# Optimization experiments

Hardware: AMD Instinct MI355X
Metric: run time of the kernel (lower is better)

Reference implementation:

```python
import jax, jax.numpy as jnp
import numpy as np

N_NODES = 100000
N_EDGES = 1600000
IN_FEATS = 128
H_FEATS = 64
NUM_CLASSES = 40
NEG_SLOPE = 0.2  # DGL GATConv default


def gat_layer(x, src, dst, W, attn_l, attn_r, bias, n_nodes):
    # x: [N, din]; W: [din, dout]; attn_l/r, bias: [dout]
    feat = x @ W                                   # [N, dout]
    el = feat @ attn_l                             # [N]
    er = feat @ attn_r                             # [N]
    e = jax.nn.leaky_relu(el[src] + er[dst], NEG_SLOPE)  # [E]
    # segment softmax over destination nodes (numerically stable)
    m = jax.ops.segment_max(e, dst, num_segments=n_nodes)   # [N]
    ee = jnp.exp(e - m[dst])                                 # [E]
    s = jax.ops.segment_sum(ee, dst, num_segments=n_nodes)  # [N]
    alpha = ee / s[dst]                                      # [E]
    out = jax.ops.segment_sum(alpha[:, None] * feat[src], dst,
                              num_segments=n_nodes)          # [N, dout]
    return out + bias


def setup_inputs() -> dict:
    key = jax.random.key(0)
    ks = jax.random.split(key, 12)
    in_feat = jax.random.normal(ks[0], (N_NODES, IN_FEATS), dtype=jnp.float32)
    src = jax.random.randint(ks[1], (N_EDGES,), 0, N_NODES, dtype=jnp.int32)
    dst = jax.random.randint(ks[2], (N_EDGES,), 0, N_NODES, dtype=jnp.int32)
    def glorot(k, shape):
        fan = sum(shape)
        return jax.random.normal(k, shape, dtype=jnp.float32) * jnp.sqrt(2.0 / fan)
    W1 = glorot(ks[3], (IN_FEATS, H_FEATS))
    al1 = glorot(ks[4], (H_FEATS,)) 
    ar1 = glorot(ks[5], (H_FEATS,))
    b1 = jnp.zeros((H_FEATS,), jnp.float32)
    W2 = glorot(ks[6], (H_FEATS, NUM_CLASSES))
    al2 = glorot(ks[7], (NUM_CLASSES,))
    ar2 = glorot(ks[8], (NUM_CLASSES,))
    b2 = jnp.zeros((NUM_CLASSES,), jnp.float32)
    return {"in_feat": in_feat, "src": src, "dst": dst,
            "W1": W1, "al1": al1, "ar1": ar1, "b1": b1,
            "W2": W2, "al2": al2, "ar2": ar2, "b2": b2}


def reference(in_feat, src, dst, W1, al1, ar1, b1, W2, al2, ar2, b2):
    h = gat_layer(in_feat, src, dst, W1, al1, ar1, b1, N_NODES)  # gat1
    h = jax.nn.elu(h)                                            # F.elu
    h = gat_layer(h, src, dst, W2, al2, ar2, b2, N_NODES)        # gat2
    return h  # [N, num_classes]
```

## Files before the change

kernel.cpp:

```cpp
#include <hip/hip_runtime.h>

#define N_NODES 100000
#define N_EDGES 1600000
#define DB_SHIFT 9
#define DB_SIZE 512
#define NDB 196
#define DB_CAP 10240
#define PART_EDGES 2048
#define NPART ((N_EDGES + PART_EDGES - 1) / PART_EDGES)
#define NGEMM1 ((N_NODES + 63) / 64)

constexpr float NEG_SLOPE = 0.2f;

__device__ __forceinline__ float leaky(float x) { return x > 0.f ? x : NEG_SLOPE * x; }

__device__ __forceinline__ float bflo(unsigned u) { return __uint_as_float(u << 16); }
__device__ __forceinline__ float bfhi(unsigned u) { return __uint_as_float(u & 0xffff0000u); }

__device__ __forceinline__ void bfsplit(float x, short& h, short& l) {
    unsigned u = __float_as_uint(x);
    h = (short)(u >> 16);
    float res = x - __uint_as_float(u & 0xffff0000u);
    unsigned r = __float_as_uint(res);
    r = (r + 0x7fffu + ((r >> 16) & 1u)) >> 16;
    l = (short)r;
}

__global__ void wconv2_kernel(const float* __restrict__ W1, const float* __restrict__ W2,
                              unsigned short* __restrict__ W1Th, unsigned short* __restrict__ W1Tl,
                              unsigned short* __restrict__ W2Th, unsigned short* __restrict__ W2Tl,
                              int* __restrict__ db_cursor) {
    int idx = blockIdx.x * 256 + threadIdx.x;
    if (blockIdx.x == 0 && threadIdx.x < NDB) db_cursor[threadIdx.x] = 0;
    if (idx < 64 * 128) {
        int n = idx / 128, k = idx % 128;
        short h, l;
        bfsplit(W1[(size_t)k * 64 + n], h, l);
        W1Th[idx] = (unsigned short)h;
        W1Tl[idx] = (unsigned short)l;
    } else if (idx < 64 * 128 + 48 * 64) {
        int j = idx - 64 * 128;
        int n = j / 64, k = j % 64;
        float x = (n < 40) ? W2[(size_t)k * 40 + n] : 0.f;
        short h, l;
        bfsplit(x, h, l);
        W2Th[j] = (unsigned short)h;
        W2Tl[j] = (unsigned short)l;
    }
}

template <int DIN, int NOUT, int NTILES, int OSTR>
__device__ __forceinline__ void gemm_mfma_body(
        int bid, const float* __restrict__ X,
        const unsigned short* __restrict__ WTh, const unsigned short* __restrict__ WTl,
        const float* __restrict__ al, const float* __restrict__ ar,
        unsigned short* __restrict__ featb, float* __restrict__ el,
        float* __restrict__ er, int N) {
    constexpr int KT = DIN / 32;
    using frag = __attribute__((ext_vector_type(8))) short;
    using accv = __attribute__((ext_vector_type(4))) float;

    int lane = threadIdx.x & 63;
    int wid = threadIdx.x >> 6;
    int r0 = (bid * 4 + wid) * 16;
    if (r0 >= N) return;
    int m = lane & 15;
    int quad = lane >> 4;
    int row = r0 + m;
    bool rok = row < N;
    const float* xrow = X + (size_t)(rok ? row : 0) * DIN;

    frag ah[KT], alo[KT];
#pragma unroll
    for (int kt = 0; kt < KT; ++kt) {
        float xv[8];
        if (rok) {
            float4 a0 = *reinterpret_cast<const float4*>(xrow + kt * 32 + quad * 8);
            float4 a1 = *reinterpret_cast<const float4*>(xrow + kt * 32 + quad * 8 + 4);
            xv[0] = a0.x; xv[1] = a0.y; xv[2] = a0.z; xv[3] = a0.w;
            xv[4] = a1.x; xv[5] = a1.y; xv[6] = a1.z; xv[7] = a1.w;
        } else {
#pragma unroll
            for (int j = 0; j < 8; ++j) xv[j] = 0.f;
        }
#pragma unroll
        for (int j = 0; j < 8; ++j) {
            short h, l;
            bfsplit(xv[j], h, l);
            ah[kt][j] = h;
            alo[kt][j] = l;
        }
    }

    accv acc[NTILES];
#pragma unroll
    for (int nt = 0; nt < NTILES; ++nt) acc[nt] = (accv){0.f, 0.f, 0.f, 0.f};

#pragma unroll
    for (int nt = 0; nt < NTILES; ++nt) {
        const unsigned short* bh_base = WTh + (size_t)(nt * 16 + m) * DIN;
        const unsigned short* bl_base = WTl + (size_t)(nt * 16 + m) * DIN;
#pragma unroll
        for (int kt = 0; kt < KT; ++kt) {
            frag bh = *reinterpret_cast<const frag*>(bh_base + kt * 32 + quad * 8);
            frag bl = *reinterpret_cast<const frag*>(bl_base + kt * 32 + quad * 8);
            acc[nt] = __builtin_amdgcn_mfma_f32_16x16x32_bf16(ah[kt], bh, acc[nt], 0, 0, 0);
            acc[nt] = __builtin_amdgcn_mfma_f32_16x16x32_bf16(ah[kt], bl, acc[nt], 0, 0, 0);
            acc[nt] = __builtin_amdgcn_mfma_f32_16x16x32_bf16(alo[kt], bh, acc[nt], 0, 0, 0);
        }
    }

    float pel[4] = {0.f, 0.f, 0.f, 0.f};
    float per[4] = {0.f, 0.f, 0.f, 0.f};
#pragma unroll
    for (int nt = 0; nt < NTILES; ++nt) {
        int n = nt * 16 + m;
        float av = (n < NOUT) ? al[n] : 0.f;
        float rv = (n < NOUT) ? ar[n] : 0.f;
#pragma unroll
        for (int reg = 0; reg < 4; ++reg) {
            float v = acc[nt][reg];
            pel[reg] += v * av;
            per[reg] += v * rv;
            int grow = r0 + quad * 4 + reg;
            if (grow < N && n < NOUT) {
                unsigned u = __float_as_uint(v);
                u = (u + 0x7fffu + ((u >> 16) & 1u)) >> 16;
                featb[(size_t)grow * OSTR + n] = (unsigned short)u;
            }
        }
    }
#pragma unroll
    for (int o = 1; o < 16; o <<= 1) {
#pragma unroll
        for (int reg = 0; reg < 4; ++reg) {
            pel[reg] += __shfl_xor(pel[reg], o, 64);
            per[reg] += __shfl_xor(per[reg], o, 64);
        }
    }
    if (m == 0) {
#pragma unroll
        for (int reg = 0; reg < 4; ++reg) {
            int grow = r0 + quad * 4 + reg;
            if (grow < N) { el[grow] = pel[reg]; er[grow] = per[reg]; }
        }
    }
}

__global__ __launch_bounds__(256) void fusedA_kernel(
        const int* __restrict__ src, const int* __restrict__ dst,
        int* __restrict__ db_cursor, unsigned* __restrict__ staged, int E,
        const float* __restrict__ X,
        const unsigned short* __restrict__ W1Th, const unsigned short* __restrict__ W1Tl,
        const float* __restrict__ al, const float* __restrict__ ar,
        unsigned short* __restrict__ featb, float* __restrict__ el,
        float* __restrict__ er, int N) {
    if (blockIdx.x < NPART) {
        __shared__ unsigned pay_s[PART_EDGES];
        __shared__ unsigned stage[PART_EDGES];
        __shared__ unsigned char bktA[PART_EDGES];
        __shared__ unsigned char bkt_s[PART_EDGES];
        __shared__ unsigned hist[256];
        __shared__ unsigned scanb[256];
        __shared__ unsigned baseg[256];
        __shared__ unsigned cnt[256];
        int tid = threadIdx.x;
        int e0 = blockIdx.x * PART_EDGES;
        hist[tid] = 0;
        cnt[tid] = 0;
        __syncthreads();
#pragma unroll
        for (int k = 0; k < PART_EDGES / 256; ++k) {
            int idx = k * 256 + tid;
            int i = e0 + idx;
            if (i < E) {
                int d = dst[i];
                unsigned b = (unsigned)d >> DB_SHIFT;
                pay_s[idx] = (((unsigned)d & (DB_SIZE - 1)) << 17) | (unsigned)src[i];
                bktA[idx] = (unsigned char)b;
                atomicAdd(&hist[b], 1u);
            }
        }
        __syncthreads();
        unsigned v = hist[tid];
        scanb[tid] = v;
        __syncthreads();
        for (int off = 1; off < 256; off <<= 1) {
            unsigned t = (tid >= off) ? scanb[tid - off] : 0;
            __syncthreads();
            scanb[tid] += t;
            __syncthreads();
        }
        unsigned excl = scanb[tid] - v;
        __syncthreads();
        scanb[tid] = excl;
        if (tid < NDB)
            baseg[tid] = (unsigned)(tid * DB_CAP) + (unsigned)atomicAdd(&db_cursor[tid], (int)v);
        __syncthreads();
#pragma unroll
        for (int k = 0; k < PART_EDGES / 256; ++k) {
            int idx = k * 256 + tid;
            int i = e0 + idx;
            if (i < E) {
                unsigned b = bktA[idx];
                unsigned slot = scanb[b] + atomicAdd(&cnt[b], 1u);
                stage[slot] = pay_s[idx];
                bkt_s[slot] = (unsigned char)b;
            }
        }
        __syncthreads();
        int total = min(PART_EDGES, E - e0);
        for (int j = tid; j < total; j += 256) {
            unsigned b = bkt_s[j];
            unsigned addr = baseg[b] + ((unsigned)j - scanb[b]);
            staged[addr] = stage[j];
        }
    } else {
        gemm_mfma_body<128, 64, 4, 64>(blockIdx.x - NPART, X, W1Th, W1Tl, al, ar, featb, el, er, N);
    }
}

__global__ __launch_bounds__(256) void bucket_sort_kernel(
        const unsigned* __restrict__ staged, const int* __restrict__ db_cursor,
        int* __restrict__ csr_src, int* __restrict__ row_ptr, int N, int E) {
    __shared__ unsigned pay[DB_CAP];
    __shared__ int sorted[DB_CAP];
    __shared__ int hist[DB_SIZE];
    __shared__ int excl[DB_SIZE];
    __shared__ int psum[256];
    __shared__ int scn[256];
    int tid = threadIdx.x;
    int k = blockIdx.x;
    int c = (tid < NDB) ? db_cursor[tid] : 0;
    scn[tid] = c;
    __syncthreads();
    for (int off = 1; off < 256; off <<= 1) {
        int t = (tid >= off) ? scn[tid - off] : 0;
        __syncthreads();
        scn[tid] += t;
        __syncthreads();
    }
    int cnt = db_cursor[k];
    int base = scn[k] - cnt;
    if (k == 0 && tid == 0) row_ptr[N] = E;

    for (int i = tid; i < DB_SIZE; i += 256) hist[i] = 0;
    __syncthreads();
    for (int j = tid; j < cnt; j += 256) {
        unsigned p = staged[(size_t)k * DB_CAP + j];
        pay[j] = p;
        atomicAdd(&hist[p >> 17], 1);
    }
    __syncthreads();
    int s = hist[2 * tid] + hist[2 * tid + 1];
    psum[tid] = s;
    __syncthreads();
    for (int off = 1; off < 256; off <<= 1) {
        int t = (tid >= off) ? psum[tid - off] : 0;
        __syncthreads();
        psum[tid] += t;
        __syncthreads();
    }
    int e0 = psum[tid] - s;
    excl[2 * tid] = e0;
    excl[2 * tid + 1] = e0 + hist[2 * tid];
    __syncthreads();
    for (int i = tid; i < DB_SIZE; i += 256) {
        int d = k * DB_SIZE + i;
        if (d < N) row_ptr[d] = base + excl[i];
    }
    for (int i = tid; i < DB_SIZE; i += 256) hist[i] = 0;
    __syncthreads();
    for (int j = tid; j < cnt; j += 256) {
        unsigned p = pay[j];
        int dl = (int)(p >> 17);
        int pos = excl[dl] + atomicAdd(&hist[dl], 1);
        sorted[pos] = (int)(p & 0x1FFFFu);
    }
    __syncthreads();
    for (int j = tid; j < cnt; j += 256) csr_src[base + j] = sorted[j];
}

__global__ __launch_bounds__(256) void gemm2_kernel(
        const float* __restrict__ X,
        const unsigned short* __restrict__ WTh, const unsigned short* __restrict__ WTl,
        const float* __restrict__ al, const float* __restrict__ ar,
        unsigned short* __restrict__ featb, float* __restrict__ el,
        float* __restrict__ er, int N) {
    gemm_mfma_body<64, 40, 3, 48>(blockIdx.x, X, WTh, WTl, al, ar, featb, el, er, N);
}

template <int DOUT, int FSTR, int OSTR, bool ELU>
__global__ void agg_kernel(const int* __restrict__ row_ptr, const int* __restrict__ csr_src,
                           const float* __restrict__ el, const float* __restrict__ er,
                           const unsigned short* __restrict__ featb,
                           const float* __restrict__ bias, float* __restrict__ outp, int N) {
    int lane = threadIdx.x & 63;
    int n = blockIdx.x * (blockDim.x >> 6) + (threadIdx.x >> 6);
    if (n >= N) return;
    int beg = row_ptr[n];
    int end = row_ptr[n + 1];
    int deg = end - beg;
    float ern = er[n];

    constexpr int G2 = DOUT / 4;

    if (deg <= 64) {
        int s = 0;
        float e = -1e30f;
        bool act = lane < deg;
        if (act) {
            s = csr_src[beg + lane];
            e = leaky(el[s] + ern);
        }
        float m = e;
#pragma unroll
        for (int o = 32; o > 0; o >>= 1) m = fmaxf(m, __shfl_xor(m, o, 64));
        float ee = act ? __expf(e - m) : 0.f;
        float ssum = ee;
#pragma unroll
        for (int o = 32; o > 0; o >>= 1) ssum += __shfl_xor(ssum, o, 64);

        int g = lane >> 4;
        int cl = lane & 15;
        float4 acc = make_float4(0.f, 0.f, 0.f, 0.f);
        int niter = (deg + 3) >> 2;
        for (int i = 0; i < niter; i += 2) {
            int e0 = 4 * i + g;
            int e1 = e0 + 4;
            float w0 = __shfl(ee, e0 & 63, 64);
            int s0 = __shfl(s, e0 & 63, 64);
            float w1 = __shfl(ee, e1 & 63, 64);
            int s1 = __shfl(s, e1 & 63, 64);
            if (e0 >= deg) w0 = 0.f;
            if (e1 >= deg) w1 = 0.f;
            if (cl < G2) {
                uint2 q0 = *(reinterpret_cast<const uint2*>(featb + (size_t)s0 * FSTR) + cl);
                uint2 q1 = *(reinterpret_cast<const uint2*>(featb + (size_t)s1 * FSTR) + cl);
                acc.x += w0 * bflo(q0.x) + w1 * bflo(q1.x);
                acc.y += w0 * bfhi(q0.x) + w1 * bfhi(q1.x);
                acc.z += w0 * bflo(q0.y) + w1 * bflo(q1.y);
                acc.w += w0 * bfhi(q0.y) + w1 * bfhi(q1.y);
            }
        }
#pragma unroll
        for (int o = 16; o <= 32; o <<= 1) {
            acc.x += __shfl_xor(acc.x, o, 64);
            acc.y += __shfl_xor(acc.y, o, 64);
            acc.z += __shfl_xor(acc.z, o, 64);
            acc.w += __shfl_xor(acc.w, o, 64);
        }
        if (g == 0 && cl < G2) {
            float inv = (deg > 0) ? 1.f / ssum : 0.f;
            const float4 b4 = reinterpret_cast<const float4*>(bias)[cl];
            float4 o4;
            o4.x = acc.x * inv + b4.x;
            o4.y = acc.y * inv + b4.y;
            o4.z = acc.z * inv + b4.z;
            o4.w = acc.w * inv + b4.w;
            if (ELU) {
                o4.x = o4.x > 0.f ? o4.x : (__expf(o4.x) - 1.f);
                o4.y = o4.y > 0.f ? o4.y : (__expf(o4.y) - 1.f);
                o4.z = o4.z > 0.f ? o4.z : (__expf(o4.z) - 1.f);
                o4.w = o4.w > 0.f ? o4.w : (__expf(o4.w) - 1.f);
            }
            *reinterpret_cast<float4*>(outp + (size_t)n * OSTR + 4 * cl) = o4;
        }
        return;
    }

    float m = -1e30f;
    for (int j = beg + lane; j < end; j += 64) {
        float e = leaky(el[csr_src[j]] + ern);
        m = fmaxf(m, e);
    }
#pragma unroll
    for (int o = 32; o > 0; o >>= 1) m = fmaxf(m, __shfl_xor(m, o, 64));

    float ssum = 0.f;
    float acc = 0.f;
    for (int base = beg; base < end; base += 64) {
        int j = base + lane;
        int cnt = min(64, end - base);
        int s = (lane < cnt) ? csr_src[j] : 0;
        float ee = 0.f;
        if (lane < cnt) {
            float e = leaky(el[s] + ern);
            ee = __expf(e - m);
        }
        ssum += ee;
        for (int t = 0; t < cnt; ++t) {
            float w = __shfl(ee, t, 64);
            int sj = __shfl(s, t, 64);
            if (lane < DOUT)
                acc += w * __uint_as_float(((unsigned)featb[(size_t)sj * FSTR + lane]) << 16);
        }
    }
#pragma unroll
    for (int o = 32; o > 0; o >>= 1) ssum += __shfl_xor(ssum, o, 64);

    if (lane < DOUT) {
        float o = acc / ssum + bias[lane];
        if (ELU) o = (o > 0.f) ? o : (__expf(o) - 1.f);
        outp[(size_t)n * OSTR + lane] = o;
    }
}

extern "C" void kernel_launch(void* const* d_in, const int* in_sizes, int n_in,
                              void* d_out, int out_size, void* d_ws, size_t ws_size,
                              hipStream_t stream) {
    const float* in_feat = (const float*)d_in[0];
    const int* src = (const int*)d_in[1];
    const int* dst = (const int*)d_in[2];
    const float* W1 = (const float*)d_in[3];
    const float* al1 = (const float*)d_in[4];
    const float* ar1 = (const float*)d_in[5];
    const float* b1 = (const float*)d_in[6];
    const float* W2 = (const float*)d_in[7];
    const float* al2 = (const float*)d_in[8];
    const float* ar2 = (const float*)d_in[9];
    const float* b2 = (const float*)d_in[10];
    float* out = (float*)d_out;

    const int N = N_NODES, E = N_EDGES;

    size_t off = 0;
    auto carve = [&](size_t bytes) {
        void* p = (char*)d_ws + off;
        off += (bytes + 255) & ~(size_t)255;
        return p;
    };
    unsigned short* featb = (unsigned short*)carve((size_t)N * 64 * 2);
    float* el    = (float*)carve((size_t)N * 4);
    float* er    = (float*)carve((size_t)N * 4);
    int* row_ptr = (int*)carve((size_t)(N + 1) * 4);
    int* csr_src = (int*)carve((size_t)E * 4);
    int* db_cursor = (int*)carve((size_t)NDB * 4);
    unsigned short* W1Th = (unsigned short*)carve((size_t)64 * 128 * 2);
    unsigned short* W1Tl = (unsigned short*)carve((size_t)64 * 128 * 2);
    unsigned short* W2Th = (unsigned short*)carve((size_t)48 * 64 * 2);
    unsigned short* W2Tl = (unsigned short*)carve((size_t)48 * 64 * 2);
    size_t offH = off;
    float* h = (float*)carve((size_t)N * 64 * 4);
    size_t off_end = off;
    off = offH;
    unsigned* staged = (unsigned*)carve((size_t)NDB * DB_CAP * 4);
    off = off_end;

    wconv2_kernel<<<(64 * 128 + 48 * 64 + 255) / 256, 256, 0, stream>>>(
        W1, W2, W1Th, W1Tl, W2Th, W2Tl, db_cursor);

    fusedA_kernel<<<NPART + NGEMM1, 256, 0, stream>>>(
        src, dst, db_cursor, staged, E,
        in_feat, W1Th, W1Tl, al1, ar1, featb, el, er, N);

    bucket_sort_kernel<<<NDB, 256, 0, stream>>>(staged, db_cursor, csr_src, row_ptr, N, E);

    int agrid = (N + 3) / 4;

    agg_kernel<64, 64, 64, true><<<agrid, 256, 0, stream>>>(row_ptr, csr_src, el, er, featb, b1, h, N);

    gemm2_kernel<<<(N + 63) / 64, 256, 0, stream>>>(h, W2Th, W2Tl, al2, ar2, featb, el, er, N);

    agg_kernel<40, 48, 40, false><<<agrid, 256, 0, stream>>>(row_ptr, csr_src, el, er, featb, b2, out, N);
}
```

Before: 288.6 us.

## Interleave partition and GEMM blocks in fused kernel; batch small-degree gathers

```diff
diff --git a/kernel.cpp b/kernel.cpp
--- a/kernel.cpp
+++ b/kernel.cpp
@@ -155,7 +155,9 @@
         const float* __restrict__ al, const float* __restrict__ ar,
         unsigned short* __restrict__ featb, float* __restrict__ el,
         float* __restrict__ er, int N) {
-    if (blockIdx.x < NPART) {
+    int p = blockIdx.x / 3;
+    int r = blockIdx.x % 3;
+    if (r == 2) {
         __shared__ unsigned pay_s[PART_EDGES];
         __shared__ unsigned stage[PART_EDGES];
         __shared__ unsigned char bktA[PART_EDGES];
@@ -165,7 +167,7 @@
         __shared__ unsigned baseg[256];
         __shared__ unsigned cnt[256];
         int tid = threadIdx.x;
-        int e0 = blockIdx.x * PART_EDGES;
+        int e0 = p * PART_EDGES;
         hist[tid] = 0;
         cnt[tid] = 0;
         __syncthreads();
@@ -216,7 +218,7 @@
             staged[addr] = stage[j];
         }
     } else {
-        gemm_mfma_body<128, 64, 4, 64>(blockIdx.x - NPART, X, W1Th, W1Tl, al, ar, featb, el, er, N);
+        gemm_mfma_body<128, 64, 4, 64>(2 * p + r, X, W1Th, W1Tl, al, ar, featb, el, er, N);
     }
 }
 
@@ -290,6 +292,34 @@
     gemm_mfma_body<64, 40, 3, 48>(blockIdx.x, X, WTh, WTl, al, ar, featb, el, er, N);
 }
 
+template <int NIT, int G2, int FSTR>
+__device__ __forceinline__ void gather_batch(int g, int cl, int s, float ee,
+                                             const unsigned short* __restrict__ featb,
+                                             float4& acc) {
+    float w[NIT];
+    int sj[NIT];
+#pragma unroll
+    for (int i = 0; i < NIT; ++i) {
+        int e = 4 * i + g;
+        w[i] = __shfl(ee, e, 64);
+        sj[i] = __shfl(s, e, 64);
+    }
+    uint2 q[NIT];
+#pragma unroll
+    for (int i = 0; i < NIT; ++i) {
+        q[i] = make_uint2(0u, 0u);
+        if (cl < G2)
+            q[i] = *(reinterpret_cast<const uint2*>(featb + (size_t)sj[i] * FSTR) + cl);
+    }
+#pragma unroll
+    for (int i = 0; i < NIT; ++i) {
+        acc.x += w[i] * bflo(q[i].x);
+        acc.y += w[i] * bfhi(q[i].x);
+        acc.z += w[i] * bflo(q[i].y);
+        acc.w += w[i] * bfhi(q[i].y);
+    }
+}
+
 template <int DOUT, int FSTR, int OSTR, bool ELU>
 __global__ void agg_kernel(const int* __restrict__ row_ptr, const int* __restrict__ csr_src,
                            const float* __restrict__ el, const float* __restrict__ er,
@@ -324,23 +354,28 @@
         int g = lane >> 4;
         int cl = lane & 15;
         float4 acc = make_float4(0.f, 0.f, 0.f, 0.f);
-        int niter = (deg + 3) >> 2;
-        for (int i = 0; i < niter; i += 2) {
-            int e0 = 4 * i + g;
-            int e1 = e0 + 4;
-            float w0 = __shfl(ee, e0 & 63, 64);
-            int s0 = __shfl(s, e0 & 63, 64);
-            float w1 = __shfl(ee, e1 & 63, 64);
-            int s1 = __shfl(s, e1 & 63, 64);
-            if (e0 >= deg) w0 = 0.f;
-            if (e1 >= deg) w1 = 0.f;
-            if (cl < G2) {
-                uint2 q0 = *(reinterpret_cast<const uint2*>(featb + (size_t)s0 * FSTR) + cl);
-                uint2 q1 = *(reinterpret_cast<const uint2*>(featb + (size_t)s1 * FSTR) + cl);
-                acc.x += w0 * bflo(q0.x) + w1 * bflo(q1.x);
-                acc.y += w0 * bfhi(q0.x) + w1 * bfhi(q1.x);
-                acc.z += w0 * bflo(q0.y) + w1 * bflo(q1.y);
-                acc.w += w0 * bfhi(q0.y) + w1 * bfhi(q1.y);
+        if (deg <= 16) {
+            gather_batch<4, G2, FSTR>(g, cl, s, ee, featb, acc);
+        } else if (deg <= 32) {
+            gather_batch<8, G2, FSTR>(g, cl, s, ee, featb, acc);
+        } else {
+            int niter = (deg + 3) >> 2;
+            for (int i = 0; i < niter; i += 2) {
+                int e0 = 4 * i + g;
+                int e1 = e0 + 4;
+                float w0 = __shfl(ee, e0 & 63, 64);
+                int s0 = __shfl(s, e0 & 63, 64);
+                float w1 = __shfl(ee, e1 & 63, 64);
+                int s1 = __shfl(s, e1 & 63, 64);
+                if (e1 >= 64) w1 = 0.f;
+                if (cl < G2) {
+                    uint2 q0 = *(reinterpret_cast<const uint2*>(featb + (size_t)s0 * FSTR) + cl);
+                    uint2 q1 = *(reinterpret_cast<const uint2*>(featb + (size_t)s1 * FSTR) + cl);
+                    acc.x += w0 * bflo(q0.x) + w1 * bflo(q1.x);
+                    acc.y += w0 * bfhi(q0.x) + w1 * bfhi(q1.x);
+                    acc.z += w0 * bflo(q0.y) + w1 * bflo(q1.y);
+                    acc.w += w0 * bfhi(q0.y) + w1 * bfhi(q1.y);
+                }
             }
         }
 #pragma unroll
@@ -450,7 +485,7 @@
     wconv2_kernel<<<(64 * 128 + 48 * 64 + 255) / 256, 256, 0, stream>>>(
         W1, W2, W1Th, W1Tl, W2Th, W2Tl, db_cursor);
 
-    fusedA_kernel<<<NPART + NGEMM1, 256, 0, stream>>>(
+    fusedA_kernel<<<3 * NPART, 256, 0, stream>>>(
         src, dst, db_cursor, staged, E,
         in_feat, W1Th, W1Tl, al1, ar1, featb, el, er, N);
 
```

After: 269.9 us. 1.07x faster.
